# Kernel tuning notes

Hardware: AMD Instinct MI355X
Metric: run time of the kernel (lower is better)

Reference implementation:

```python
import jax, jax.numpy as jnp
import numpy as np

B, NPOS, NNEG, D, NLEM = 8, 512, 512, 128, 32768
MOMENTUM = 0.5
EPS = 1e-12  # F.normalize eps


def setup_inputs() -> dict:
    key = jax.random.key(0)
    k1, k2, k3, k4 = jax.random.split(key, 4)
    x = jax.random.normal(k1, (B, NPOS + NNEG, D), dtype=jnp.float32)
    y = jax.random.randint(k2, (B, NPOS), 0, NPOS).astype(jnp.int64)
    visible = jax.random.randint(k3, (B, NPOS), 0, 2).astype(jnp.int32)
    stdv = 1.0 / np.sqrt(D / 3.0)
    memory = jax.random.uniform(k4, (NLEM, D), dtype=jnp.float32,
                                minval=-stdv, maxval=stdv)
    return {"x": x, "y": y, "visible": visible, "memory": memory, "lru": 3}


def reference(x, y, visible, memory, lru):
    # --- similarity computation (differentiable path) ---
    t = x[:, :NPOS, :]                                  # [B, NPOS, D]
    similarity = jnp.einsum('bpd,md->bpm', t, memory)    # [B, NPOS, NLEM]
    noise_similarity = jnp.einsum('bnd,pd->bnp',
                                  x[:, NPOS:, :], memory[:NPOS])  # [B, NNEG, NPOS]
    y_idx = y.astype(jnp.int64)

    # --- memory bank update (no-grad in original) ---
    vis = visible.astype(x.dtype)[..., None]             # [B, NPOS, 1]
    get = jnp.mean(t * vis, axis=0)                      # [NPOS, D]
    pos_new = memory[:NPOS] * MOMENTUM + get * (1.0 - MOMENTUM)
    neg_flat = x[:, NPOS:, :].reshape(-1, D)             # [B*NNEG, D]
    start = NPOS + lru * NNEG * B                        # lru is a python int
    new_mem = memory.at[start:start + NNEG * B].set(neg_flat)
    new_mem = new_mem.at[:NPOS].set(pos_new)
    norms = jnp.maximum(jnp.linalg.norm(new_mem, axis=1, keepdims=True), EPS)
    new_mem = jax.lax.stop_gradient(new_mem / norms)

    return similarity, y_idx, noise_similarity, new_mem
```

## Files before the change

### kernel.cpp

```cpp
#include <hip/hip_runtime.h>
#include <hip/hip_bf16.h>
#include <cstdint>

#define NPOS 512
#define NNEG 512
#define BATCH 8
#define DDIM 128
#define NLEM 32768
#define NX_ELEM (BATCH * (NPOS + NNEG) * DDIM)
#define NM_ELEM (NLEM * DDIM)
#define NK_STEPS 32

typedef __attribute__((ext_vector_type(4))) float f32x4;
typedef __attribute__((ext_vector_type(16))) float f32x16;
typedef __attribute__((ext_vector_type(8))) short short8;

__device__ __forceinline__ unsigned short f2bf(float f) {
  unsigned u = __float_as_uint(f);
  u = (u + 0x7FFFu + ((u >> 16) & 1u)) >> 16;
  return (unsigned short)u;
}

__device__ __forceinline__ short8 cvt8(f32x4 a0, f32x4 a1) {
  short8 w;
  w[0] = (short)f2bf(a0[0]); w[1] = (short)f2bf(a0[1]);
  w[2] = (short)f2bf(a0[2]); w[3] = (short)f2bf(a0[3]);
  w[4] = (short)f2bf(a1[0]); w[5] = (short)f2bf(a1[1]);
  w[6] = (short)f2bf(a1[2]); w[7] = (short)f2bf(a1[3]);
  return w;
}

__device__ __forceinline__ void async16(const void* g, void* l) {
  __builtin_amdgcn_global_load_lds(
      (const __attribute__((address_space(1))) unsigned int*)g,
      (__attribute__((address_space(3))) unsigned int*)l, 16, 0, 0);
}

__device__ __forceinline__ void newmem_row(int r, int lane, const float* __restrict__ X,
                                           const int* __restrict__ vis,
                                           const float* __restrict__ Mem, int start,
                                           float* __restrict__ out) {
  const int d0 = lane, d1 = lane + 64;
  float v0, v1;
  if (r < NPOS) {
    const float s0 = Mem[(size_t)r * DDIM + d0];
    const float s1 = Mem[(size_t)r * DDIM + d1];
    float a0 = 0.f, a1 = 0.f;
#pragma unroll
    for (int b = 0; b < BATCH; ++b) {
      const float w = (float)vis[b * NPOS + r];
      const float* px = X + (size_t)(b * (NPOS + NNEG) + r) * DDIM;
      a0 += w * px[d0];
      a1 += w * px[d1];
    }
    v0 = 0.5f * s0 + 0.0625f * a0;
    v1 = 0.5f * s1 + 0.0625f * a1;
  } else if (r >= start && r < start + BATCH * NNEG) {
    const int q = r - start;
    const int b = q >> 9, n = q & 511;
    const float* px = X + (size_t)(b * (NPOS + NNEG) + NPOS + n) * DDIM;
    v0 = px[d0];
    v1 = px[d1];
  } else {
    v0 = Mem[(size_t)r * DDIM + d0];
    v1 = Mem[(size_t)r * DDIM + d1];
  }
  float s = v0 * v0 + v1 * v1;
#pragma unroll
  for (int off = 32; off; off >>= 1) s += __shfl_xor(s, off, 64);
  const float inv = 1.0f / fmaxf(sqrtf(s), 1e-12f);
  out[(size_t)r * DDIM + d0] = v0 * inv;
  out[(size_t)r * DDIM + d1] = v1 * inv;
}

__global__ __launch_bounds__(256) void prep_kernel(
    const float* __restrict__ X, const int* __restrict__ y,
    const int* __restrict__ vis, const float* __restrict__ Mem,
    const int* __restrict__ lru_p, unsigned short* __restrict__ xb,
    unsigned short* __restrict__ mb, float* __restrict__ out_y,
    float* __restrict__ out_mem) {
  const int blk = blockIdx.x;
  if (blk < 256) {
    const size_t i = (size_t)(blk >> 5) * 131072 + (size_t)(blk & 31) * 2048 +
                     (size_t)threadIdx.x * 8;
    *(short8*)(xb + i) = cvt8(*(const f32x4*)(X + i), *(const f32x4*)(X + i + 4));
  } else if (blk < 2304) {
    const size_t i = ((size_t)(blk - 256) * 256 + threadIdx.x) * 8;
    *(short8*)(mb + i) = cvt8(*(const f32x4*)(Mem + i), *(const f32x4*)(Mem + i + 4));
  } else if (blk < 2320) {
    const int i = (blk - 2304) * 256 + threadIdx.x;
    out_y[i] = (float)y[i];
  } else {
    const int r = (blk - 2320) * 4 + (threadIdx.x >> 6);
    const int start = NPOS + lru_p[0] * (NNEG * BATCH);
    newmem_row(r, threadIdx.x & 63, X, vis, Mem, start, out_mem);
  }
}

__global__ __launch_bounds__(256, 1) void gemm_band_kernel(
    const unsigned short* __restrict__ Xb, const unsigned short* __restrict__ Mb,
    float* __restrict__ Csim) {
  __shared__ short ldsA[2][128 * 128];
  __shared__ short ldsB[128 * 128];

  const int t = threadIdx.x;
  const int lane = t & 63, wv = t >> 6;
  const int rl = lane >> 4, slot = lane & 15;
  const int wr = wv >> 1, wc = wv & 1;
  const int la = lane & 31, lb = lane >> 5;
  const int b = blockIdx.x;
  const int n0 = b * 128;

  auto stageA = [&](int p, int k) {
    const int m0 = k * 128;
    const int xbase = ((m0 >> 9) << 10) + (m0 & 511);
#pragma unroll
    for (int i = 0; i < 8; ++i) {
      const int rowb = wv * 32 + i * 4;
      const int row = rowb + rl;
      const int ss = slot ^ (row & 15);
      async16(Xb + (size_t)(xbase + row) * DDIM + ss * 8, &ldsA[p][rowb * 128]);
    }
  };

#pragma unroll
  for (int i = 0; i < 8; ++i) {
    const int rowb = wv * 32 + i * 4;
    const int row = rowb + rl;
    const int ss = slot ^ (row & 15);
    async16(Mb + (size_t)(n0 + row) * DDIM + ss * 8, &ldsB[rowb * 128]);
  }
  stageA(0, 0);
  asm volatile("s_waitcnt vmcnt(0)" ::: "memory");
  __builtin_amdgcn_s_barrier();
  __builtin_amdgcn_sched_barrier(0);

  short8 bfr[8][2];
#pragma unroll
  for (int kk = 0; kk < 8; ++kk)
#pragma unroll
    for (int n2 = 0; n2 < 2; ++n2) {
      const int row = wc * 64 + n2 * 32 + la;
      const int ss = ((kk * 2 + lb) ^ (row & 15)) * 8;
      bfr[kk][n2] = *(const short8*)&ldsB[row * 128 + ss];
    }

  int p = 0;
  for (int k = 0; k < NK_STEPS; ++k) {
    if (k + 1 < NK_STEPS) stageA(p ^ 1, k + 1);

    f32x16 acc[2][2] = {};
#pragma unroll
    for (int kk = 0; kk < 8; ++kk) {
      short8 af[2];
#pragma unroll
      for (int m2 = 0; m2 < 2; ++m2) {
        const int row = wr * 64 + m2 * 32 + la;
        const int ss = ((kk * 2 + lb) ^ (row & 15)) * 8;
        af[m2] = *(const short8*)&ldsA[p][row * 128 + ss];
      }
#pragma unroll
      for (int m2 = 0; m2 < 2; ++m2)
#pragma unroll
        for (int n2 = 0; n2 < 2; ++n2)
          acc[m2][n2] = __builtin_amdgcn_mfma_f32_32x32x16_bf16(
              af[m2], bfr[kk][n2], acc[m2][n2], 0, 0, 0);
    }

    const int m0 = k * 128;
#pragma unroll
    for (int m2 = 0; m2 < 2; ++m2) {
#pragma unroll
      for (int n2 = 0; n2 < 2; ++n2) {
        const int col = n0 + wc * 64 + n2 * 32 + la;
        const int rbase = m0 + wr * 64 + m2 * 32 + lb * 4;
#pragma unroll
        for (int r = 0; r < 16; ++r) {
          const int row = rbase + (r & 3) + 8 * (r >> 2);
          Csim[(size_t)row * NLEM + col] = acc[m2][n2][r];
        }
      }
    }

    if (k + 1 < NK_STEPS) {
      asm volatile("s_waitcnt vmcnt(60)" ::: "memory");
      __builtin_amdgcn_s_barrier();
      __builtin_amdgcn_sched_barrier(0);
    }
    p ^= 1;
  }
}

__global__ __launch_bounds__(256) void gemm_conv_kernel(
    const float* __restrict__ X, const float* __restrict__ Bm,
    float* __restrict__ C, int ldc, int a_off) {
  __shared__ short lds[2 * 128 * 128];
  short* ldsA = lds;
  short* ldsB = lds + 128 * 128;
  const int t = threadIdx.x;
  const int m0 = blockIdx.x * 128;
  const int n0 = blockIdx.y * 128;
  const int slot = t & 15;
  const int rsub = t >> 4;
#pragma unroll
  for (int it = 0; it < 8; ++it) {
    const int row = it * 16 + rsub;
    const int gr = m0 + row;
    const int xrow = ((gr >> 9) << 10) + (gr & 511) + a_off;
    const f32x4* pa = (const f32x4*)(X + (size_t)xrow * DDIM + slot * 8);
    const f32x4* pb = (const f32x4*)(Bm + (size_t)(n0 + row) * DDIM + slot * 8);
    short8 wa = cvt8(pa[0], pa[1]);
    short8 wb = cvt8(pb[0], pb[1]);
    const int ss = (slot ^ (row & 15)) * 8;
    *(short8*)&ldsA[row * 128 + ss] = wa;
    *(short8*)&ldsB[row * 128 + ss] = wb;
  }
  __syncthreads();
  const int lane = t & 63;
  const int wv = t >> 6;
  const int wr = wv >> 1, wc = wv & 1;
  const int la = lane & 31, lb = lane >> 5;
  f32x16 acc[2][2] = {};
#pragma unroll
  for (int kk = 0; kk < 8; ++kk) {
    short8 af[2], bfr[2];
#pragma unroll
    for (int m2 = 0; m2 < 2; ++m2) {
      const int row = wr * 64 + m2 * 32 + la;
      const int ss = ((kk * 2 + lb) ^ (row & 15)) * 8;
      af[m2] = *(const short8*)&ldsA[row * 128 + ss];
    }
#pragma unroll
    for (int n2 = 0; n2 < 2; ++n2) {
      const int row = wc * 64 + n2 * 32 + la;
      const int ss = ((kk * 2 + lb) ^ (row & 15)) * 8;
      bfr[n2] = *(const short8*)&ldsB[row * 128 + ss];
    }
#pragma unroll
    for (int m2 = 0; m2 < 2; ++m2)
#pragma unroll
      for (int n2 = 0; n2 < 2; ++n2)
        acc[m2][n2] = __builtin_amdgcn_mfma_f32_32x32x16_bf16(
            af[m2], bfr[n2], acc[m2][n2], 0, 0, 0);
  }
#pragma unroll
  for (int m2 = 0; m2 < 2; ++m2)
#pragma unroll
    for (int n2 = 0; n2 < 2; ++n2) {
      const int col = n0 + wc * 64 + n2 * 32 + la;
      const int rbase = m0 + wr * 64 + m2 * 32 + lb * 4;
#pragma unroll
      for (int r = 0; r < 16; ++r) {
        const int row = rbase + (r & 3) + 8 * (r >> 2);
        C[(size_t)row * ldc + col] = acc[m2][n2][r];
      }
    }
}

__global__ void y_kernel(const int* __restrict__ y, float* __restrict__ out) {
  const int i = blockIdx.x * blockDim.x + threadIdx.x;
  if (i < BATCH * NPOS) out[i] = (float)y[i];
}

__global__ __launch_bounds__(256) void newmem_kernel(
    const float* __restrict__ X, const int* __restrict__ vis,
    const float* __restrict__ Mem, const int* __restrict__ lru_p,
    float* __restrict__ out) {
  const int r = blockIdx.x * 4 + (threadIdx.x >> 6);
  const int start = NPOS + lru_p[0] * (NNEG * BATCH);
  newmem_row(r, threadIdx.x & 63, X, vis, Mem, start, out);
}

extern "C" void kernel_launch(void* const* d_in, const int* in_sizes, int n_in,
                              void* d_out, int out_size, void* d_ws, size_t ws_size,
                              hipStream_t stream) {
  const float* x = (const float*)d_in[0];
  const int* y = (const int*)d_in[1];
  const int* visible = (const int*)d_in[2];
  const float* memory = (const float*)d_in[3];
  const int* lru = (const int*)d_in[4];
  float* out = (float*)d_out;

  const size_t OFF_Y = (size_t)BATCH * NPOS * NLEM;
  const size_t OFF_NOISE = OFF_Y + (size_t)BATCH * NPOS;
  const size_t OFF_MEM = OFF_NOISE + (size_t)BATCH * NNEG * NPOS;

  const size_t need = (size_t)(NX_ELEM + NM_ELEM) * 2;
  if (ws_size >= need) {
    unsigned short* xb = (unsigned short*)d_ws;
    unsigned short* mb = xb + NX_ELEM;
    gemm_conv_kernel<<<dim3(32, 4), 256, 0, stream>>>(x, memory, out + OFF_NOISE, NPOS, NPOS);
    prep_kernel<<<10512, 256, 0, stream>>>(
        x, y, visible, memory, lru, xb, mb, out + OFF_Y, out + OFF_MEM);
    gemm_band_kernel<<<256, 256, 0, stream>>>(xb, mb, out);
  } else {
    gemm_conv_kernel<<<dim3(32, 256), 256, 0, stream>>>(x, memory, out, NLEM, 0);
    gemm_conv_kernel<<<dim3(32, 4), 256, 0, stream>>>(x, memory, out + OFF_NOISE, NPOS, NPOS);
    y_kernel<<<16, 256, 0, stream>>>(y, out + OFF_Y);
    newmem_kernel<<<NLEM / 4, 256, 0, stream>>>(x, visible, memory, lru, out + OFF_MEM);
  }
}
```

Measured before the change: 125.7 us.

## Fuse bf16 conversion and memory-bank update into the band GEMM kernel

Removes the separate prep kernel that wrote bf16 copies of X and memory to workspace. The band GEMM now loads fp32 panels into registers, converts them to bf16 and stores them swizzled into LDS, prefetching the next A panel while the current one is computed. After the GEMM, each block also computes its 128 normalized new-memory rows and its share of the y cast. Similarity outputs are written with nontemporal stores. This saves a kernel launch and a workspace round trip, but costs more registers (about 64 extra floats) and puts the conversion on the GEMM critical path.

```diff
diff --git a/kernel.cpp b/kernel.cpp
--- a/kernel.cpp
+++ b/kernel.cpp
@@ -7,8 +7,6 @@
 #define BATCH 8
 #define DDIM 128
 #define NLEM 32768
-#define NX_ELEM (BATCH * (NPOS + NNEG) * DDIM)
-#define NM_ELEM (NLEM * DDIM)
 #define NK_STEPS 32
 
 typedef __attribute__((ext_vector_type(4))) float f32x4;
@@ -28,12 +26,6 @@
   w[4] = (short)f2bf(a1[0]); w[5] = (short)f2bf(a1[1]);
   w[6] = (short)f2bf(a1[2]); w[7] = (short)f2bf(a1[3]);
   return w;
-}
-
-__device__ __forceinline__ void async16(const void* g, void* l) {
-  __builtin_amdgcn_global_load_lds(
-      (const __attribute__((address_space(1))) unsigned int*)g,
-      (__attribute__((address_space(3))) unsigned int*)l, 16, 0, 0);
 }
 
 __device__ __forceinline__ void newmem_row(int r, int lane, const float* __restrict__ X,
@@ -73,65 +65,50 @@
   out[(size_t)r * DDIM + d1] = v1 * inv;
 }
 
-__global__ __launch_bounds__(256) void prep_kernel(
+__global__ __launch_bounds__(256, 1) void fused_kernel(
     const float* __restrict__ X, const int* __restrict__ y,
     const int* __restrict__ vis, const float* __restrict__ Mem,
-    const int* __restrict__ lru_p, unsigned short* __restrict__ xb,
-    unsigned short* __restrict__ mb, float* __restrict__ out_y,
-    float* __restrict__ out_mem) {
-  const int blk = blockIdx.x;
-  if (blk < 256) {
-    const size_t i = (size_t)(blk >> 5) * 131072 + (size_t)(blk & 31) * 2048 +
-                     (size_t)threadIdx.x * 8;
-    *(short8*)(xb + i) = cvt8(*(const f32x4*)(X + i), *(const f32x4*)(X + i + 4));
-  } else if (blk < 2304) {
-    const size_t i = ((size_t)(blk - 256) * 256 + threadIdx.x) * 8;
-    *(short8*)(mb + i) = cvt8(*(const f32x4*)(Mem + i), *(const f32x4*)(Mem + i + 4));
-  } else if (blk < 2320) {
-    const int i = (blk - 2304) * 256 + threadIdx.x;
-    out_y[i] = (float)y[i];
-  } else {
-    const int r = (blk - 2320) * 4 + (threadIdx.x >> 6);
-    const int start = NPOS + lru_p[0] * (NNEG * BATCH);
-    newmem_row(r, threadIdx.x & 63, X, vis, Mem, start, out_mem);
-  }
-}
-
-__global__ __launch_bounds__(256, 1) void gemm_band_kernel(
-    const unsigned short* __restrict__ Xb, const unsigned short* __restrict__ Mb,
-    float* __restrict__ Csim) {
+    const int* __restrict__ lru_p, float* __restrict__ Csim,
+    float* __restrict__ out_y, float* __restrict__ out_mem) {
   __shared__ short ldsA[2][128 * 128];
   __shared__ short ldsB[128 * 128];
 
   const int t = threadIdx.x;
   const int lane = t & 63, wv = t >> 6;
-  const int rl = lane >> 4, slot = lane & 15;
   const int wr = wv >> 1, wc = wv & 1;
   const int la = lane & 31, lb = lane >> 5;
   const int b = blockIdx.x;
   const int n0 = b * 128;
 
-  auto stageA = [&](int p, int k) {
-    const int m0 = k * 128;
-    const int xbase = ((m0 >> 9) << 10) + (m0 & 511);
-#pragma unroll
-    for (int i = 0; i < 8; ++i) {
-      const int rowb = wv * 32 + i * 4;
-      const int row = rowb + rl;
-      const int ss = slot ^ (row & 15);
-      async16(Xb + (size_t)(xbase + row) * DDIM + ss * 8, &ldsA[p][rowb * 128]);
-    }
+  const int srow = t >> 1;
+  const int scol = (t & 1) * 64;
+  const int sslot0 = scol >> 3;
+
+  auto apanel = [&](int k) -> const float* {
+    return X + ((size_t)(k >> 2) * 1024 + (size_t)(k & 3) * 128) * DDIM;
   };
 
-#pragma unroll
-  for (int i = 0; i < 8; ++i) {
-    const int rowb = wv * 32 + i * 4;
-    const int row = rowb + rl;
-    const int ss = slot ^ (row & 15);
-    async16(Mb + (size_t)(n0 + row) * DDIM + ss * 8, &ldsB[rowb * 128]);
-  }
-  stageA(0, 0);
-  asm volatile("s_waitcnt vmcnt(0)" ::: "memory");
+  auto cvt_store = [&](const f32x4* v, short* dst) {
+#pragma unroll
+    for (int j = 0; j < 8; ++j) {
+      short8 w = cvt8(v[2 * j], v[2 * j + 1]);
+      const int ss = (sslot0 + j) ^ (srow & 15);
+      *(short8*)&dst[srow * 128 + ss * 8] = w;
+    }
+  };
+
+  {
+    f32x4 vb[16], va[16];
+    const f32x4* pb = (const f32x4*)(Mem + (size_t)(n0 + srow) * DDIM + scol);
+    const f32x4* pa = (const f32x4*)(apanel(0) + (size_t)srow * DDIM + scol);
+#pragma unroll
+    for (int j = 0; j < 16; ++j) vb[j] = pb[j];
+#pragma unroll
+    for (int j = 0; j < 16; ++j) va[j] = pa[j];
+    cvt_store(vb, ldsB);
+    cvt_store(va, ldsA[0]);
+  }
+  asm volatile("s_waitcnt lgkmcnt(0)" ::: "memory");
   __builtin_amdgcn_s_barrier();
   __builtin_amdgcn_sched_barrier(0);
 
@@ -147,7 +124,12 @@
 
   int p = 0;
   for (int k = 0; k < NK_STEPS; ++k) {
-    if (k + 1 < NK_STEPS) stageA(p ^ 1, k + 1);
+    f32x4 vnext[16];
+    if (k + 1 < NK_STEPS) {
+      const f32x4* pn = (const f32x4*)(apanel(k + 1) + (size_t)srow * DDIM + scol);
+#pragma unroll
+      for (int j = 0; j < 16; ++j) vnext[j] = pn[j];
+    }
 
     f32x16 acc[2][2] = {};
 #pragma unroll
@@ -177,18 +159,26 @@
 #pragma unroll
         for (int r = 0; r < 16; ++r) {
           const int row = rbase + (r & 3) + 8 * (r >> 2);
-          Csim[(size_t)row * NLEM + col] = acc[m2][n2][r];
+          __builtin_nontemporal_store(acc[m2][n2][r],
+                                      &Csim[(size_t)row * NLEM + col]);
         }
       }
     }
 
     if (k + 1 < NK_STEPS) {
-      asm volatile("s_waitcnt vmcnt(60)" ::: "memory");
+      cvt_store(vnext, ldsA[p ^ 1]);
+      asm volatile("s_waitcnt lgkmcnt(0)" ::: "memory");
       __builtin_amdgcn_s_barrier();
       __builtin_amdgcn_sched_barrier(0);
     }
     p ^= 1;
   }
+
+  const int start = NPOS + lru_p[0] * (NNEG * BATCH);
+#pragma unroll 1
+  for (int i = 0; i < 32; ++i)
+    newmem_row(b * 128 + wv * 32 + i, lane, X, vis, Mem, start, out_mem);
+  if (t < 16) out_y[b * 16 + t] = (float)y[b * 16 + t];
 }
 
 __global__ __launch_bounds__(256) void gemm_conv_kernel(
@@ -257,20 +247,6 @@
     }
 }
 
-__global__ void y_kernel(const int* __restrict__ y, float* __restrict__ out) {
-  const int i = blockIdx.x * blockDim.x + threadIdx.x;
-  if (i < BATCH * NPOS) out[i] = (float)y[i];
-}
-
-__global__ __launch_bounds__(256) void newmem_kernel(
-    const float* __restrict__ X, const int* __restrict__ vis,
-    const float* __restrict__ Mem, const int* __restrict__ lru_p,
-    float* __restrict__ out) {
-  const int r = blockIdx.x * 4 + (threadIdx.x >> 6);
-  const int start = NPOS + lru_p[0] * (NNEG * BATCH);
-  newmem_row(r, threadIdx.x & 63, X, vis, Mem, start, out);
-}
-
 extern "C" void kernel_launch(void* const* d_in, const int* in_sizes, int n_in,
                               void* d_out, int out_size, void* d_ws, size_t ws_size,
                               hipStream_t stream) {
@@ -285,18 +261,8 @@
   const size_t OFF_NOISE = OFF_Y + (size_t)BATCH * NPOS;
   const size_t OFF_MEM = OFF_NOISE + (size_t)BATCH * NNEG * NPOS;
 
-  const size_t need = (size_t)(NX_ELEM + NM_ELEM) * 2;
-  if (ws_size >= need) {
-    unsigned short* xb = (unsigned short*)d_ws;
-    unsigned short* mb = xb + NX_ELEM;
-    gemm_conv_kernel<<<dim3(32, 4), 256, 0, stream>>>(x, memory, out + OFF_NOISE, NPOS, NPOS);
-    prep_kernel<<<10512, 256, 0, stream>>>(
-        x, y, visible, memory, lru, xb, mb, out + OFF_Y, out + OFF_MEM);
-    gemm_band_kernel<<<256, 256, 0, stream>>>(xb, mb, out);
-  } else {
-    gemm_conv_kernel<<<dim3(32, 256), 256, 0, stream>>>(x, memory, out, NLEM, 0);
-    gemm_conv_kernel<<<dim3(32, 4), 256, 0, stream>>>(x, memory, out + OFF_NOISE, NPOS, NPOS);
-    y_kernel<<<16, 256, 0, stream>>>(y, out + OFF_Y);
-    newmem_kernel<<<NLEM / 4, 256, 0, stream>>>(x, visible, memory, lru, out + OFF_MEM);
-  }
-}
+  gemm_conv_kernel<<<dim3(32, 4), 256, 0, stream>>>(x, memory, out + OFF_NOISE,
+                                                    NPOS, NPOS);
+  fused_kernel<<<256, 256, 0, stream>>>(x, y, visible, memory, lru, out,
+                                        out + OFF_Y, out + OFF_MEM);
+}
```

Measured after the change: 166.4 us. 32.4% more time.

## Fuse noise GEMM and memory normalization into band GEMM kernel

Applied to the files above, without the earlier changes.

Merges the noise-similarity GEMM and the new-memory normalization into the main band GEMM kernel, so the fast path issues two launches instead of three. The B tile of memory is now converted from fp32 to bf16 inside the GEMM kernel, so the prep kernel only converts x and the first 512 memory rows. This cuts the bf16 workspace traffic for the full memory bank and saves launch overhead. The cost is an extra tail of serial normalization work in each GEMM block, which runs after the stores and could lengthen the critical path, plus an unbalanced noise tile handled only by the first 128 blocks.

```diff
diff --git a/kernel.cpp b/kernel.cpp
--- a/kernel.cpp
+++ b/kernel.cpp
@@ -8,7 +8,7 @@
 #define DDIM 128
 #define NLEM 32768
 #define NX_ELEM (BATCH * (NPOS + NNEG) * DDIM)
-#define NM_ELEM (NLEM * DDIM)
+#define NM512_ELEM (NPOS * DDIM)
 #define NK_STEPS 32
 
 typedef __attribute__((ext_vector_type(4))) float f32x4;
@@ -75,31 +75,73 @@
 
 __global__ __launch_bounds__(256) void prep_kernel(
     const float* __restrict__ X, const int* __restrict__ y,
-    const int* __restrict__ vis, const float* __restrict__ Mem,
-    const int* __restrict__ lru_p, unsigned short* __restrict__ xb,
-    unsigned short* __restrict__ mb, float* __restrict__ out_y,
+    const float* __restrict__ Mem, unsigned short* __restrict__ xb,
+    unsigned short* __restrict__ mb512, float* __restrict__ out_y) {
+  const int blk = blockIdx.x;
+  if (blk < 512) {
+    const size_t i = ((size_t)blk * 256 + threadIdx.x) * 8;
+    *(short8*)(xb + i) = cvt8(*(const f32x4*)(X + i), *(const f32x4*)(X + i + 4));
+  } else if (blk < 544) {
+    const size_t i = ((size_t)(blk - 512) * 256 + threadIdx.x) * 8;
+    *(short8*)(mb512 + i) = cvt8(*(const f32x4*)(Mem + i), *(const f32x4*)(Mem + i + 4));
+  } else {
+    const int i = (blk - 544) * 256 + threadIdx.x;
+    out_y[i] = (float)y[i];
+  }
+}
+
+__device__ __forceinline__ void tile_compute_store(
+    const short* Atile, const short8 bfr[8][2], float* __restrict__ C, int ldc,
+    int m0, int n0c, int wr, int wc, int la, int lb) {
+  f32x16 acc[2][2] = {};
+#pragma unroll
+  for (int kk = 0; kk < 8; ++kk) {
+    short8 af[2];
+#pragma unroll
+    for (int m2 = 0; m2 < 2; ++m2) {
+      const int row = wr * 64 + m2 * 32 + la;
+      const int ss = ((kk * 2 + lb) ^ (row & 15)) * 8;
+      af[m2] = *(const short8*)&Atile[row * 128 + ss];
+    }
+#pragma unroll
+    for (int m2 = 0; m2 < 2; ++m2)
+#pragma unroll
+      for (int n2 = 0; n2 < 2; ++n2)
+        acc[m2][n2] = __builtin_amdgcn_mfma_f32_32x32x16_bf16(
+            af[m2], bfr[kk][n2], acc[m2][n2], 0, 0, 0);
+  }
+#pragma unroll
+  for (int m2 = 0; m2 < 2; ++m2)
+#pragma unroll
+    for (int n2 = 0; n2 < 2; ++n2) {
+      const int col = n0c + wc * 64 + n2 * 32 + la;
+      const int rbase = m0 + wr * 64 + m2 * 32 + lb * 4;
+#pragma unroll
+      for (int r = 0; r < 16; ++r) {
+        const int row = rbase + (r & 3) + 8 * (r >> 2);
+        C[(size_t)row * ldc + col] = acc[m2][n2][r];
+      }
+    }
+}
+
+__device__ __forceinline__ void hoist_b(const short* Btile, short8 bfr[8][2],
+                                        int wc, int la, int lb) {
+#pragma unroll
+  for (int kk = 0; kk < 8; ++kk)
+#pragma unroll
+    for (int n2 = 0; n2 < 2; ++n2) {
+      const int row = wc * 64 + n2 * 32 + la;
+      const int ss = ((kk * 2 + lb) ^ (row & 15)) * 8;
+      bfr[kk][n2] = *(const short8*)&Btile[row * 128 + ss];
+    }
+}
+
+__global__ __launch_bounds__(256, 1) void fused_kernel(
+    const float* __restrict__ X, const int* __restrict__ vis,
+    const float* __restrict__ Mem, const int* __restrict__ lru_p,
+    const unsigned short* __restrict__ xb, const unsigned short* __restrict__ mb512,
+    float* __restrict__ Csim, float* __restrict__ Cnoise,
     float* __restrict__ out_mem) {
-  const int blk = blockIdx.x;
-  if (blk < 256) {
-    const size_t i = (size_t)(blk >> 5) * 131072 + (size_t)(blk & 31) * 2048 +
-                     (size_t)threadIdx.x * 8;
-    *(short8*)(xb + i) = cvt8(*(const f32x4*)(X + i), *(const f32x4*)(X + i + 4));
-  } else if (blk < 2304) {
-    const size_t i = ((size_t)(blk - 256) * 256 + threadIdx.x) * 8;
-    *(short8*)(mb + i) = cvt8(*(const f32x4*)(Mem + i), *(const f32x4*)(Mem + i + 4));
-  } else if (blk < 2320) {
-    const int i = (blk - 2304) * 256 + threadIdx.x;
-    out_y[i] = (float)y[i];
-  } else {
-    const int r = (blk - 2320) * 4 + (threadIdx.x >> 6);
-    const int start = NPOS + lru_p[0] * (NNEG * BATCH);
-    newmem_row(r, threadIdx.x & 63, X, vis, Mem, start, out_mem);
-  }
-}
-
-__global__ __launch_bounds__(256, 1) void gemm_band_kernel(
-    const unsigned short* __restrict__ Xb, const unsigned short* __restrict__ Mb,
-    float* __restrict__ Csim) {
   __shared__ short ldsA[2][128 * 128];
   __shared__ short ldsB[128 * 128];
 
@@ -111,84 +153,70 @@
   const int b = blockIdx.x;
   const int n0 = b * 128;
 
-  auto stageA = [&](int p, int k) {
-    const int m0 = k * 128;
-    const int xbase = ((m0 >> 9) << 10) + (m0 & 511);
+  auto stage_tile = [&](short* dst, const unsigned short* src, int rowbase) {
 #pragma unroll
     for (int i = 0; i < 8; ++i) {
       const int rowb = wv * 32 + i * 4;
       const int row = rowb + rl;
       const int ss = slot ^ (row & 15);
-      async16(Xb + (size_t)(xbase + row) * DDIM + ss * 8, &ldsA[p][rowb * 128]);
+      async16(src + (size_t)(rowbase + row) * DDIM + ss * 8, &dst[rowb * 128]);
     }
   };
 
-#pragma unroll
-  for (int i = 0; i < 8; ++i) {
-    const int rowb = wv * 32 + i * 4;
-    const int row = rowb + rl;
-    const int ss = slot ^ (row & 15);
-    async16(Mb + (size_t)(n0 + row) * DDIM + ss * 8, &ldsB[rowb * 128]);
-  }
-  stageA(0, 0);
-  asm volatile("s_waitcnt vmcnt(0)" ::: "memory");
+  stage_tile(ldsA[0], xb, 0);
+  {
+    const int srow = t >> 1, scol = (t & 1) * 64, sslot0 = scol >> 3;
+    f32x4 vb[16];
+    const f32x4* pb = (const f32x4*)(Mem + (size_t)(n0 + srow) * DDIM + scol);
+#pragma unroll
+    for (int j = 0; j < 16; ++j) vb[j] = pb[j];
+#pragma unroll
+    for (int j = 0; j < 8; ++j) {
+      short8 w = cvt8(vb[2 * j], vb[2 * j + 1]);
+      const int ss = (sslot0 + j) ^ (srow & 15);
+      *(short8*)&ldsB[srow * 128 + ss * 8] = w;
+    }
+  }
+  asm volatile("s_waitcnt vmcnt(0) lgkmcnt(0)" ::: "memory");
   __builtin_amdgcn_s_barrier();
   __builtin_amdgcn_sched_barrier(0);
 
   short8 bfr[8][2];
-#pragma unroll
-  for (int kk = 0; kk < 8; ++kk)
-#pragma unroll
-    for (int n2 = 0; n2 < 2; ++n2) {
-      const int row = wc * 64 + n2 * 32 + la;
-      const int ss = ((kk * 2 + lb) ^ (row & 15)) * 8;
-      bfr[kk][n2] = *(const short8*)&ldsB[row * 128 + ss];
-    }
+  hoist_b(ldsB, bfr, wc, la, lb);
 
   int p = 0;
   for (int k = 0; k < NK_STEPS; ++k) {
-    if (k + 1 < NK_STEPS) stageA(p ^ 1, k + 1);
-
-    f32x16 acc[2][2] = {};
-#pragma unroll
-    for (int kk = 0; kk < 8; ++kk) {
-      short8 af[2];
-#pragma unroll
-      for (int m2 = 0; m2 < 2; ++m2) {
-        const int row = wr * 64 + m2 * 32 + la;
-        const int ss = ((kk * 2 + lb) ^ (row & 15)) * 8;
-        af[m2] = *(const short8*)&ldsA[p][row * 128 + ss];
-      }
-#pragma unroll
-      for (int m2 = 0; m2 < 2; ++m2)
-#pragma unroll
-        for (int n2 = 0; n2 < 2; ++n2)
-          acc[m2][n2] = __builtin_amdgcn_mfma_f32_32x32x16_bf16(
-              af[m2], bfr[kk][n2], acc[m2][n2], 0, 0, 0);
-    }
-
-    const int m0 = k * 128;
-#pragma unroll
-    for (int m2 = 0; m2 < 2; ++m2) {
-#pragma unroll
-      for (int n2 = 0; n2 < 2; ++n2) {
-        const int col = n0 + wc * 64 + n2 * 32 + la;
-        const int rbase = m0 + wr * 64 + m2 * 32 + lb * 4;
-#pragma unroll
-        for (int r = 0; r < 16; ++r) {
-          const int row = rbase + (r & 3) + 8 * (r >> 2);
-          Csim[(size_t)row * NLEM + col] = acc[m2][n2][r];
-        }
-      }
-    }
-
     if (k + 1 < NK_STEPS) {
+      const int kn = k + 1;
+      stage_tile(ldsA[p ^ 1], xb, (kn >> 2) * 1024 + (kn & 3) * 128);
+    } else if (b < 128) {
+      const int rp = b >> 2, cb = b & 3;
+      stage_tile(ldsA[p ^ 1], xb, (rp >> 2) * 1024 + 512 + (rp & 3) * 128);
+      stage_tile(ldsB, mb512, cb * 128);
+    }
+
+    tile_compute_store(ldsA[p], bfr, Csim, NLEM, k * 128, n0, wr, wc, la, lb);
+
+    if (k + 1 < NK_STEPS || b < 128) {
       asm volatile("s_waitcnt vmcnt(60)" ::: "memory");
       __builtin_amdgcn_s_barrier();
       __builtin_amdgcn_sched_barrier(0);
     }
     p ^= 1;
   }
+
+  if (b < 128) {
+    const int rp = b >> 2, cb = b & 3;
+    short8 bfr2[8][2];
+    hoist_b(ldsB, bfr2, wc, la, lb);
+    tile_compute_store(ldsA[p], bfr2, Cnoise, NPOS, rp * 128, cb * 128,
+                       wr, wc, la, lb);
+  }
+
+  const int start = NPOS + lru_p[0] * (NNEG * BATCH);
+#pragma unroll 1
+  for (int i = 0; i < 32; ++i)
+    newmem_row(b * 128 + wv * 32 + i, lane, X, vis, Mem, start, out_mem);
 }
 
 __global__ __launch_bounds__(256) void gemm_conv_kernel(
@@ -220,41 +248,9 @@
   const int wv = t >> 6;
   const int wr = wv >> 1, wc = wv & 1;
   const int la = lane & 31, lb = lane >> 5;
-  f32x16 acc[2][2] = {};
-#pragma unroll
-  for (int kk = 0; kk < 8; ++kk) {
-    short8 af[2], bfr[2];
-#pragma unroll
-    for (int m2 = 0; m2 < 2; ++m2) {
-      const int row = wr * 64 + m2 * 32 + la;
-      const int ss = ((kk * 2 + lb) ^ (row & 15)) * 8;
-      af[m2] = *(const short8*)&ldsA[row * 128 + ss];
-    }
-#pragma unroll
-    for (int n2 = 0; n2 < 2; ++n2) {
-      const int row = wc * 64 + n2 * 32 + la;
-      const int ss = ((kk * 2 + lb) ^ (row & 15)) * 8;
-      bfr[n2] = *(const short8*)&ldsB[row * 128 + ss];
-    }
-#pragma unroll
-    for (int m2 = 0; m2 < 2; ++m2)
-#pragma unroll
-      for (int n2 = 0; n2 < 2; ++n2)
-        acc[m2][n2] = __builtin_amdgcn_mfma_f32_32x32x16_bf16(
-            af[m2], bfr[n2], acc[m2][n2], 0, 0, 0);
-  }
-#pragma unroll
-  for (int m2 = 0; m2 < 2; ++m2)
-#pragma unroll
-    for (int n2 = 0; n2 < 2; ++n2) {
-      const int col = n0 + wc * 64 + n2 * 32 + la;
-      const int rbase = m0 + wr * 64 + m2 * 32 + lb * 4;
-#pragma unroll
-      for (int r = 0; r < 16; ++r) {
-        const int row = rbase + (r & 3) + 8 * (r >> 2);
-        C[(size_t)row * ldc + col] = acc[m2][n2][r];
-      }
-    }
+  short8 bfr[8][2];
+  hoist_b(ldsB, bfr, wc, la, lb);
+  tile_compute_store(ldsA, bfr, C, ldc, m0, n0, wr, wc, la, lb);
 }
 
 __global__ void y_kernel(const int* __restrict__ y, float* __restrict__ out) {
@@ -285,14 +281,13 @@
   const size_t OFF_NOISE = OFF_Y + (size_t)BATCH * NPOS;
   const size_t OFF_MEM = OFF_NOISE + (size_t)BATCH * NNEG * NPOS;
 
-  const size_t need = (size_t)(NX_ELEM + NM_ELEM) * 2;
+  const size_t need = (size_t)(NX_ELEM + NM512_ELEM) * 2;
   if (ws_size >= need) {
     unsigned short* xb = (unsigned short*)d_ws;
-    unsigned short* mb = xb + NX_ELEM;
-    gemm_conv_kernel<<<dim3(32, 4), 256, 0, stream>>>(x, memory, out + OFF_NOISE, NPOS, NPOS);
-    prep_kernel<<<10512, 256, 0, stream>>>(
-        x, y, visible, memory, lru, xb, mb, out + OFF_Y, out + OFF_MEM);
-    gemm_band_kernel<<<256, 256, 0, stream>>>(xb, mb, out);
+    unsigned short* mb512 = xb + NX_ELEM;
+    prep_kernel<<<560, 256, 0, stream>>>(x, y, memory, xb, mb512, out + OFF_Y);
+    fused_kernel<<<256, 256, 0, stream>>>(x, visible, memory, lru, xb, mb512,
+                                          out, out + OFF_NOISE, out + OFF_MEM);
   } else {
     gemm_conv_kernel<<<dim3(32, 256), 256, 0, stream>>>(x, memory, out, NLEM, 0);
     gemm_conv_kernel<<<dim3(32, 4), 256, 0, stream>>>(x, memory, out + OFF_NOISE, NPOS, NPOS);
```

Measured after the change: 154.1 us. 1.23x slower.
